# Optimization experiments

Hardware: AMD Instinct MI355X
Metric: run time of the kernel (lower is better)

## Reference

```python
import jax, jax.numpy as jnp
import numpy as np
from jax import lax

# dims (see shape_source)
B, C, H, W = 2, 128, 48, 48
HEADS = 4
G = 4                 # offset_groups = heads
DH = C // HEADS       # 32, dim_head
DF = 4                # downsample_factor
OKS = 6               # offset_kernel_size
PAD = (OKS - DF) // 2 # 1
OFFSET_SCALE = 4.0
CPB_DIM = C // 4      # 32
OD = C // G           # offset_dims = 32


def setup_inputs() -> dict:
    key = jax.random.key(0)
    ks = jax.random.split(key, 12)
    rn = lambda k, shape, s=0.05: jax.random.normal(k, shape, dtype=jnp.float32) * s
    return {
        "x": jax.random.normal(ks[0], (B, C, H, W), dtype=jnp.float32),
        "gamma": jax.random.normal(ks[1], (1,), dtype=jnp.float32),  # nn.Parameter([0.0]); randomized so both paths contribute
        "wq": rn(ks[2], (G, DH, C // G)),    # grouped 1x1 conv, groups=G
        "wk": rn(ks[3], (G, DH, C // G)),
        "wv": rn(ks[4], (G, DH, C // G)),
        "wo": rn(ks[5], (C, C)),             # to_out 1x1 conv
        "bo": jnp.zeros((C,), jnp.float32),
        "w_off_dw": rn(ks[6], (OD, 1, OKS, OKS)),  # depthwise conv k=6 s=4 p=1
        "b_off_dw": jnp.zeros((OD,), jnp.float32),
        "w_off_proj": rn(ks[7], (2, OD)),          # 1x1 conv to 2 offset channels, no bias
        "cpb_w0": rn(ks[8], (2, CPB_DIM), 0.5),
        "cpb_b0": jnp.zeros((CPB_DIM,), jnp.float32),
        "cpb_w1": rn(ks[9], (CPB_DIM, CPB_DIM), 0.2),
        "cpb_b1": jnp.zeros((CPB_DIM,), jnp.float32),
        "cpb_w2": rn(ks[10], (CPB_DIM, HEADS // G), 0.2),
        "cpb_b2": jnp.zeros((HEADS // G,), jnp.float32),
    }


def _bilinear_sample(img, px, py):
    """F.grid_sample(mode='bilinear', padding_mode='zeros') on pixel coords.
    img: (N, Cg, Hi, Wi); px, py: (N, Ho, Wo) -> (N, Cg, Ho, Wo)"""
    N, Cg, Hi, Wi = img.shape
    imgf = img.reshape(N, Cg, Hi * Wi)
    x0 = jnp.floor(px)
    y0 = jnp.floor(py)
    wx1 = px - x0
    wy1 = py - y0

    def corner(xc, yc, w):
        valid = (xc >= 0) & (xc <= Wi - 1) & (yc >= 0) & (yc <= Hi - 1)
        xi = jnp.clip(xc, 0, Wi - 1).astype(jnp.int32)
        yi = jnp.clip(yc, 0, Hi - 1).astype(jnp.int32)
        idx = (yi * Wi + xi).reshape(N, -1)
        vals = jnp.take_along_axis(imgf, idx[:, None, :], axis=2)  # (N,Cg,Ho*Wo)
        return vals * (w * valid).reshape(N, 1, -1)

    out = (corner(x0, y0, (1 - wx1) * (1 - wy1))
           + corner(x0 + 1, y0, wx1 * (1 - wy1))
           + corner(x0, y0 + 1, (1 - wx1) * wy1)
           + corner(x0 + 1, y0 + 1, wx1 * wy1))
    return out.reshape(N, Cg, px.shape[1], px.shape[2])


def _forward(x, gamma, wq, wk, wv, wo, bo, w_off_dw, b_off_dw, w_off_proj,
             cpb_w0, cpb_b0, cpb_w1, cpb_b1, cpb_w2, cpb_b2):
    b = x.shape[0]
    scale = DH ** -0.5
    xg = x.reshape(b, G, C // G, H, W)
    # grouped 1x1 conv -> queries (b, G, DH, H, W); channel layout (g d) == (h d) since G==HEADS
    q = jnp.einsum('bgchw,goc->bgohw', xg, wq)
    gq = q.reshape(b * G, DH, H, W)
    # to_offsets: depthwise conv (k=6, s=4, p=1) -> GELU -> 1x1 to 2ch -> tanh -> *offset_scale
    off = lax.conv_general_dilated(gq, w_off_dw, (DF, DF), [(PAD, PAD), (PAD, PAD)],
                                   feature_group_count=OD,
                                   dimension_numbers=('NCHW', 'OIHW', 'NCHW'))
    off = jax.nn.gelu(off + b_off_dw[None, :, None, None], approximate=False)
    off = jnp.tanh(jnp.einsum('bchw,oc->bohw', off, w_off_proj)) * OFFSET_SCALE  # (bG,2,Hd,Wd)
    Hd, Wd = off.shape[-2], off.shape[-1]
    gy, gx = jnp.meshgrid(jnp.arange(Hd, dtype=jnp.float32),
                          jnp.arange(Wd, dtype=jnp.float32), indexing='ij')
    vg0 = gx[None] + off[:, 0]  # channel 0 = x (meshgrid 'xy' in torch code)
    vg1 = gy[None] + off[:, 1]  # channel 1 = y
    vn0 = 2.0 * vg0 / max(Hd - 1, 1) - 1.0  # normalize_grid (H==W so h/w quirk is moot)
    vn1 = 2.0 * vg1 / max(Wd - 1, 1) - 1.0
    # grid_sample align_corners=False unnormalization: pix = ((u+1)*size - 1)/2
    px = ((vn0 + 1.0) * W - 1.0) / 2.0
    py = ((vn1 + 1.0) * H - 1.0) / 2.0
    kv = _bilinear_sample(xg.reshape(b * G, C // G, H, W), px, py)  # (bG, C/G, Hd, Wd)
    kvg = kv.reshape(b, G, C // G, Hd, Wd)
    k = jnp.einsum('bgchw,goc->bgohw', kvg, wk)
    v = jnp.einsum('bgchw,goc->bgohw', kvg, wv)
    i, j = H * W, Hd * Wd
    qh = q.reshape(b, HEADS, DH, i).transpose(0, 1, 3, 2) * scale  # (b,h,i,d)
    kh = k.reshape(b, HEADS, DH, j).transpose(0, 1, 3, 2)
    vh = v.reshape(b, HEADS, DH, j).transpose(0, 1, 3, 2)
    sim = jnp.einsum('bhid,bhjd->bhij', qh, kh)
    # CPB relative position bias
    gyq, gxq = jnp.meshgrid(jnp.arange(H, dtype=jnp.float32),
                            jnp.arange(W, dtype=jnp.float32), indexing='ij')
    qn0 = 2.0 * gxq / max(H - 1, 1) - 1.0
    qn1 = 2.0 * gyq / max(W - 1, 1) - 1.0
    grid_q = jnp.stack([qn0, qn1], -1).reshape(1, i, 1, 2)
    grid_kv = jnp.stack([vn0, vn1], -1).reshape(b * G, 1, j, 2)
    pos = grid_q - grid_kv                       # (bG, i, j, 2)
    bias = jnp.sign(pos) * jnp.log1p(jnp.abs(pos))
    h1 = jax.nn.relu(bias @ cpb_w0 + cpb_b0)
    h2 = jax.nn.relu(h1 @ cpb_w1 + cpb_b1)
    bias = h2 @ cpb_w2 + cpb_b2                  # (bG, i, j, heads//G)
    bias = bias.reshape(b, G, i, j, HEADS // G).transpose(0, 1, 4, 2, 3).reshape(b, HEADS, i, j)
    attn = jax.nn.softmax(sim + bias, axis=-1)
    outh = jnp.einsum('bhij,bhjd->bhid', attn, vh)
    out = outh.transpose(0, 1, 3, 2).reshape(b, C, H, W)  # 'b h (x y) d -> b (h d) x y'
    attention = jnp.einsum('bchw,oc->bohw', out, wo) + bo[None, :, None, None]
    return gamma[0] * attention + x, attention


def reference(x, gamma, wq, wk, wv, wo, bo, w_off_dw, b_off_dw, w_off_proj,
              cpb_w0, cpb_b0, cpb_w1, cpb_b1, cpb_w2, cpb_b2):
    return _forward(x, gamma, wq, wk, wv, wo, bo, w_off_dw, b_off_dw, w_off_proj,
                    cpb_w0, cpb_b0, cpb_w1, cpb_b1, cpb_w2, cpb_b2)
```

## Files before the change

### kernel.cpp

```cpp
#include <hip/hip_runtime.h>
#include <math.h>

#define HWHW 2304
#define JD   144
#define LSP  148

typedef __attribute__((ext_vector_type(8))) short short8;
typedef __attribute__((ext_vector_type(4))) float f32x4;
typedef __attribute__((ext_vector_type(2))) float f32x2;

__device__ inline ushort f2bf(float f) {
  uint u = __float_as_uint(f);
  u += 0x7fffu + ((u >> 16) & 1u);
  return (ushort)(u >> 16);
}
__device__ inline float bf2f(ushort s) { return __uint_as_float((uint)s << 16); }
__device__ inline uint packbf(float hi, float lo) {
  return __builtin_amdgcn_perm(__float_as_uint(hi), __float_as_uint(lo), 0x07060302);
}


__global__ __launch_bounds__(384) void offset_kv_kernel(
    const float* __restrict__ x, const float* __restrict__ wq,
    const float* __restrict__ wdw, const float* __restrict__ bdw,
    const float* __restrict__ wproj, const float* __restrict__ wk,
    const float* __restrict__ wv,
    ushort* __restrict__ ktb, ushort* __restrict__ vtb,
    float* __restrict__ S0g, float* __restrict__ S1g) {
  __shared__ float qs[288][33];
  __shared__ float wdws[36][32];
  __shared__ float wkl[32][33], wvl[32][33];
  __shared__ float kvs[32][13];
  __shared__ float spx[12], spy[12];
  __shared__ float spn0[12], spn1[12];
  int hd = blockIdx.x, bg = blockIdx.y, b = bg >> 2, g = bg & 3;
  int t = threadIdx.x;
  int w = t >> 6, lane = t & 63, lam = lane & 15, quad = lane >> 4;

  {
    int hy = hd * 4 - 1 + w;
    if (hy >= 0 && hy < 48) {
      const float* wqg = wq + (g * 32) * 32;
      float4 wa = *(const float4*)(wqg + lam * 32 + quad * 8);
      float4 wb = *(const float4*)(wqg + lam * 32 + quad * 8 + 4);
      float4 wc = *(const float4*)(wqg + (16 + lam) * 32 + quad * 8);
      float4 wd = *(const float4*)(wqg + (16 + lam) * 32 + quad * 8 + 4);
      union { uint u[4]; short8 s8; } bf0, bf1;
      bf0.u[0] = packbf(wa.y, wa.x); bf0.u[1] = packbf(wa.w, wa.z);
      bf0.u[2] = packbf(wb.y, wb.x); bf0.u[3] = packbf(wb.w, wb.z);
      bf1.u[0] = packbf(wc.y, wc.x); bf1.u[1] = packbf(wc.w, wc.z);
      bf1.u[2] = packbf(wd.y, wd.x); bf1.u[3] = packbf(wd.w, wd.z);
      const float* xg = x + (b * 128 + g * 32) * HWHW + hy * 48;
#pragma unroll
      for (int tt = 0; tt < 3; ++tt) {
        int col = tt * 16 + lam;
        union { uint u[4]; short8 s8; } xa;
#pragma unroll
        for (int j = 0; j < 4; ++j) {
          float x0 = xg[(quad * 8 + 2 * j) * HWHW + col];
          float x1 = xg[(quad * 8 + 2 * j + 1) * HWHW + col];
          xa.u[j] = packbf(x1, x0);
        }
        f32x4 z = {0.f, 0.f, 0.f, 0.f};
        f32x4 d0 = __builtin_amdgcn_mfma_f32_16x16x32_bf16(xa.s8, bf0.s8, z, 0, 0, 0);
        f32x4 d1 = __builtin_amdgcn_mfma_f32_16x16x32_bf16(xa.s8, bf1.s8, z, 0, 0, 0);
        int p = w * 48 + tt * 16 + quad * 4;
#pragma unroll
        for (int r = 0; r < 4; ++r) {
          qs[p + r][lam] = d0[r];
          qs[p + r][16 + lam] = d1[r];
        }
      }
    } else {
#pragma unroll
      for (int tt = 0; tt < 3; ++tt) {
        int p = w * 48 + tt * 16 + quad * 4;
#pragma unroll
        for (int r = 0; r < 4; ++r) {
          qs[p + r][lam] = 0.f;
          qs[p + r][16 + lam] = 0.f;
        }
      }
    }
  }
  for (int u = t; u < 1152; u += 384) wdws[u >> 5][u & 31] = wdw[(u & 31) * 36 + (u >> 5)];
  for (int u = t; u < 1024; u += 384) {
    int d = u >> 5, c = u & 31;
    wkl[d][c] = wk[g * 1024 + u];
    wvl[d][c] = wv[g * 1024 + u];
  }
  __syncthreads();
  {
    int wd = t >> 5, c = t & 31;
    float s = 0.f;
#pragma unroll
    for (int ky = 0; ky < 6; ++ky) {
#pragma unroll
      for (int kx = 0; kx < 6; ++kx) {
        int wx = wd * 4 - 1 + kx;
        if (wx >= 0 && wx < 48)
          s += wdws[ky * 6 + kx][c] * qs[ky * 48 + wx][c];
      }
    }
    s += bdw[c];
    s = 0.5f * s * (1.f + erff(s * 0.70710678118654752f));
    float g0 = wproj[c] * s;
    float g1 = wproj[32 + c] * s;
#pragma unroll
    for (int k = 16; k >= 1; k >>= 1) {
      g0 += __shfl_xor(g0, k, 64);
      g1 += __shfl_xor(g1, k, 64);
    }
    if (c == 0) {
      float off0 = tanhf(g0) * 4.f;
      float off1 = tanhf(g1) * 4.f;
      float n0 = 2.f * ((float)wd + off0) / 11.f - 1.f;
      float n1 = 2.f * ((float)hd + off1) / 11.f - 1.f;
      spn0[wd] = n0;
      spn1[wd] = n1;
      spx[wd] = ((n0 + 1.f) * 48.f - 1.f) * 0.5f;
      spy[wd] = ((n1 + 1.f) * 48.f - 1.f) * 0.5f;
    }
  }
  __syncthreads();
  {
    int j = t >> 5, c = t & 31;
    float fx = spx[j], fy = spy[j];
    float x0 = floorf(fx), y0 = floorf(fy);
    float wx = fx - x0, wy = fy - y0;
    int xi = (int)x0, yi = (int)y0;
    const float* xp = x + (b * 128 + g * 32 + c) * HWHW;
    float v00 = 0.f, v10 = 0.f, v01 = 0.f, v11 = 0.f;
    bool okx0 = (xi >= 0) & (xi < 48), okx1 = (xi + 1 >= 0) & (xi + 1 < 48);
    if (yi >= 0 && yi < 48) {
      if (okx0) v00 = xp[yi * 48 + xi];
      if (okx1) v10 = xp[yi * 48 + xi + 1];
    }
    if (yi + 1 >= 0 && yi + 1 < 48) {
      if (okx0) v01 = xp[(yi + 1) * 48 + xi];
      if (okx1) v11 = xp[(yi + 1) * 48 + xi + 1];
    }
    kvs[c][j] = v00 * (1.f - wx) * (1.f - wy) + v10 * wx * (1.f - wy)
              + v01 * (1.f - wx) * wy + v11 * wx * wy;
  }
  {
#pragma unroll
    for (int it = 0; it < 3; ++it) {
      int u = t + it * 384;
      int tab = u >= 576;
      int idx = tab ? u - 576 : u;
      int ii = idx / 12, wd = idx - ii * 12;
      float qn = (float)ii * (2.f / 47.f) - 1.f;
      float nv = tab ? spn1[wd] : spn0[wd];
      float p = qn - nv;
      float sres = copysignf(__logf(1.f + fabsf(p)), p);
      float* dst = tab ? S1g : S0g;
      dst[bg * 6912 + ii * 144 + hd * 12 + wd] = sres;
    }
  }
  __syncthreads();
  {
    int j = t >> 5, d = t & 31;
    float ak = 0.f, av = 0.f;
#pragma unroll
    for (int c = 0; c < 32; ++c) {
      float val = kvs[c][j];
      ak += wkl[d][c] * val;
      av += wvl[d][c] * val;
    }
    int jg = hd * 12 + j;
    ktb[bg * 4608 + jg * 32 + d] = f2bf(ak);
    vtb[bg * 5120 + d * 160 + jg] = f2bf(av);
  }
  if (hd == 0) {
    for (int u = t; u < 512; u += 384)
      vtb[bg * 5120 + (u >> 4) * 160 + 144 + (u & 15)] = 0;
  }
}

__global__ __launch_bounds__(256) void attn_fused_kernel(
    const float* __restrict__ x, const float* __restrict__ wq,
    const ushort* __restrict__ ktb, const ushort* __restrict__ vtb,
    const float* __restrict__ S0g, const float* __restrict__ S1g,
    const float* __restrict__ w0, const float* __restrict__ b0,
    const float* __restrict__ w1, const float* __restrict__ b1,
    const float* __restrict__ w2, const float* __restrict__ b2,
    ushort* __restrict__ outh) {
  __shared__ __align__(16) char smem[20288];
  float* Ls = (float*)smem;
  float* st0f = (float*)(smem + 9472);
  float* st1f = (float*)(smem + 18688);
  ushort* qbf = (ushort*)(smem + 19264);

  int bg = blockIdx.y, b = bg >> 2, g = bg & 3;
  int i0 = blockIdx.x * 16;
  int t = threadIdx.x;
  int w = t >> 6, lane = t & 63;
  int lam = lane & 15, quad = lane >> 4;

  {
    int iy = i0 / 48;
    int ix0 = i0 - iy * 48;
    const float* S0p = S0g + bg * 6912 + ix0 * 144;
#pragma unroll
    for (int it = 0; it < 9; ++it) st0f[t + it * 256] = S0p[t + it * 256];
    if (t < JD) st1f[t] = S1g[bg * 6912 + iy * 144 + t];
  }

  {
    const float* wqg = wq + (g * 32) * 32;
    float4 wa = *(const float4*)(wqg + lam * 32 + quad * 8);
    float4 wb = *(const float4*)(wqg + lam * 32 + quad * 8 + 4);
    float4 wc = *(const float4*)(wqg + (16 + lam) * 32 + quad * 8);
    float4 wd = *(const float4*)(wqg + (16 + lam) * 32 + quad * 8 + 4);
    union { uint u[4]; short8 s8; } bf0, bf1, xa;
    bf0.u[0] = packbf(wa.y, wa.x); bf0.u[1] = packbf(wa.w, wa.z);
    bf0.u[2] = packbf(wb.y, wb.x); bf0.u[3] = packbf(wb.w, wb.z);
    bf1.u[0] = packbf(wc.y, wc.x); bf1.u[1] = packbf(wc.w, wc.z);
    bf1.u[2] = packbf(wd.y, wd.x); bf1.u[3] = packbf(wd.w, wd.z);
    const float* xg = x + (b * 128 + g * 32) * HWHW + i0;
#pragma unroll
    for (int j = 0; j < 4; ++j) {
      float x0 = xg[(quad * 8 + 2 * j) * HWHW + lam];
      float x1 = xg[(quad * 8 + 2 * j + 1) * HWHW + lam];
      xa.u[j] = packbf(x1, x0);
    }
    f32x4 z = {0.f, 0.f, 0.f, 0.f};
    f32x4 d0 = __builtin_amdgcn_mfma_f32_16x16x32_bf16(xa.s8, bf0.s8, z, 0, 0, 0);
    f32x4 d1 = __builtin_amdgcn_mfma_f32_16x16x32_bf16(xa.s8, bf1.s8, z, 0, 0, 0);
#pragma unroll
    for (int r = 0; r < 4; ++r) {
      qbf[(quad * 4 + r) * 32 + lam] = f2bf(d0[r]);
      qbf[(quad * 4 + r) * 32 + 16 + lam] = f2bf(d1[r]);
    }
  }

  f32x2 w00r2[4], w01r2[4], b0r2[4];
#pragma unroll
  for (int j = 0; j < 4; ++j) {
    int k = quad * 8 + 2 * j;
    w00r2[j] = (f32x2){w0[k], w0[k + 1]};
    w01r2[j] = (f32x2){w0[32 + k], w0[32 + k + 1]};
    b0r2[j]  = (f32x2){b0[k], b0[k + 1]};
  }
  short8 w1f0, w1f1;
#pragma unroll
  for (int j = 0; j < 8; ++j) {
    int k = quad * 8 + j;
    w1f0[j] = (short)f2bf(w1[k * 32 + lam]);
    w1f1[j] = (short)f2bf(w1[k * 32 + 16 + lam]);
  }
  f32x4 zA, zB;
  f32x2 w2A01, w2A23, w2B01, w2B23;
#pragma unroll
  for (int r = 0; r < 4; ++r) {
    zA[r] = b1[quad * 4 + r];
    zB[r] = b1[16 + quad * 4 + r];
  }
  w2A01 = (f32x2){w2[quad * 4], w2[quad * 4 + 1]};
  w2A23 = (f32x2){w2[quad * 4 + 2], w2[quad * 4 + 3]};
  w2B01 = (f32x2){w2[16 + quad * 4], w2[16 + quad * 4 + 1]};
  w2B23 = (f32x2){w2[16 + quad * 4 + 2], w2[16 + quad * 4 + 3]};
  float b2s = b2[0];

  short8 vf[5];
  if (w < 2) {
    const ushort* vb = vtb + bg * 5120 + (w * 16 + lam) * 160;
#pragma unroll
    for (int kb = 0; kb < 5; ++kb)
      vf[kb] = *(const short8*)(vb + kb * 32 + quad * 8);
  }

  __syncthreads();

  const float scale = 0.17677669529663687f;
  {
    short8 aq = *(const short8*)(qbf + lam * 32 + quad * 8);
    const ushort* kb = ktb + bg * 4608;
#pragma unroll 1
    for (int jt = w; jt < 9; jt += 4) {
      short8 bk = *(const short8*)(kb + (jt * 16 + lam) * 32 + quad * 8);
      f32x4 acc = {0.f, 0.f, 0.f, 0.f};
      acc = __builtin_amdgcn_mfma_f32_16x16x32_bf16(aq, bk, acc, 0, 0, 0);
#pragma unroll
      for (int r = 0; r < 4; ++r)
        Ls[(quad * 4 + r) * LSP + jt * 16 + lam] = acc[r] * scale;
    }
  }
  __syncthreads();

  const f32x2 zero2 = {0.f, 0.f};
  int pbase = w * 576;
#pragma unroll 1
  for (int s = 0; s < 9; ++s) {
    float bm[4];
#pragma unroll
    for (int mt = 0; mt < 4; ++mt) {
      int Pm = pbase + s * 64 + mt * 16 + lam;
      float s0 = st0f[Pm];
      int iim = Pm / 144;
      float s1 = st1f[Pm - iim * 144];
      f32x2 s0v = {s0, s0}, s1v = {s1, s1};
      union { uint u[4]; short8 s8; } cvt;
#pragma unroll
      for (int j = 0; j < 4; ++j) {
        f32x2 hv = __builtin_elementwise_max(
            __builtin_elementwise_fma(s0v, w00r2[j],
                __builtin_elementwise_fma(s1v, w01r2[j], b0r2[j])), zero2);
        cvt.u[j] = packbf(hv[1], hv[0]);
      }
      f32x4 dA = __builtin_amdgcn_mfma_f32_16x16x32_bf16(w1f0, cvt.s8, zA, 0, 0, 0);
      f32x4 dB = __builtin_amdgcn_mfma_f32_16x16x32_bf16(w1f1, cvt.s8, zB, 0, 0, 0);
      f32x2 a01 = __builtin_elementwise_max((f32x2){dA[0], dA[1]}, zero2);
      f32x2 a23 = __builtin_elementwise_max((f32x2){dA[2], dA[3]}, zero2);
      f32x2 c01 = __builtin_elementwise_max((f32x2){dB[0], dB[1]}, zero2);
      f32x2 c23 = __builtin_elementwise_max((f32x2){dB[2], dB[3]}, zero2);
      f32x2 av = __builtin_elementwise_fma(a01, w2A01,
                 __builtin_elementwise_fma(a23, w2A23,
                 __builtin_elementwise_fma(c01, w2B01,
                 __builtin_elementwise_fma(c23, w2B23, zero2))));
      float acc = av[0] + av[1];
      acc += __shfl_xor(acc, 16, 64);
      acc += __shfl_xor(acc, 32, 64);
      bm[mt] = acc;
    }
    int P = s * 64 + lane;
    int ii = P / 144, jj = P - ii * 144;
    float biasv = (quad == 0 ? bm[0] : quad == 1 ? bm[1] : quad == 2 ? bm[2] : bm[3]) + b2s;
    Ls[(w * 4 + ii) * LSP + jj] += biasv;
  }
  __syncthreads();

  {
    int row = w * 4 + quad;
    float* Lp = Ls + row * LSP;
    float lv[9];
#pragma unroll
    for (int k = 0; k < 9; ++k) lv[k] = Lp[lam + 16 * k];
    float m = lv[0];
#pragma unroll
    for (int k = 1; k < 9; ++k) m = fmaxf(m, lv[k]);
#pragma unroll
    for (int k = 8; k >= 1; k >>= 1) m = fmaxf(m, __shfl_xor(m, k, 64));
    float e[9], sum = 0.f;
#pragma unroll
    for (int k = 0; k < 9; ++k) { e[k] = __expf(lv[k] - m); sum += e[k]; }
#pragma unroll
    for (int k = 8; k >= 1; k >>= 1) sum += __shfl_xor(sum, k, 64);
    float inv = 1.f / sum;
    ushort* pb = (ushort*)(Lp + 64);
#pragma unroll
    for (int k = 0; k < 9; ++k) pb[lam + 16 * k] = f2bf(e[k] * inv);
    pb[144 + lam] = 0;
  }
  __syncthreads();

  if (w < 2) {
    f32x4 o = {0.f, 0.f, 0.f, 0.f};
    const ushort* pb = (const ushort*)(Ls + lam * LSP + 64);
#pragma unroll
    for (int kb = 0; kb < 5; ++kb) {
      short8 ap = *(const short8*)(pb + kb * 32 + quad * 8);
      o = __builtin_amdgcn_mfma_f32_16x16x32_bf16(ap, vf[kb], o, 0, 0, 0);
    }
#pragma unroll
    for (int r = 0; r < 4; ++r) {
      int ig = i0 + quad * 4 + r;
      outh[((long)b * HWHW + ig) * 128 + g * 32 + w * 16 + lam] = f2bf(o[r]);
    }
  }
}

__global__ __launch_bounds__(256) void out_kernel(
    const ushort* __restrict__ outh, const float* __restrict__ wo,
    const float* __restrict__ bo, const float* __restrict__ x,
    const float* __restrict__ gamma, float* __restrict__ out) {
  int b = blockIdx.y;
  int hw0 = blockIdx.x * 16;
  int oc0 = blockIdx.z * 64;
  int t = threadIdx.x;
  int w = t >> 6, lane = t & 63, lam = lane & 15, quad = lane >> 4;
  const ushort* abase = outh + ((long)b * HWHW + hw0 + lam) * 128 + quad * 8;
  const float* wb0 = wo + (oc0 + w * 16 + lam) * 128 + quad * 8;
  f32x4 acc0 = {0.f, 0.f, 0.f, 0.f};
#pragma unroll
  for (int ks = 0; ks < 4; ++ks) {
    short8 a = *(const short8*)(abase + ks * 32);
    float4 wa = *(const float4*)(wb0 + ks * 32);
    float4 wb = *(const float4*)(wb0 + ks * 32 + 4);
    union { uint u[4]; short8 s8; } p0;
    p0.u[0] = packbf(wa.y, wa.x); p0.u[1] = packbf(wa.w, wa.z);
    p0.u[2] = packbf(wb.y, wb.x); p0.u[3] = packbf(wb.w, wb.z);
    acc0 = __builtin_amdgcn_mfma_f32_16x16x32_bf16(a, p0.s8, acc0, 0, 0, 0);
  }
  float gm = gamma[0];
  float* out0 = out;
  float* out1 = out + 2 * 128 * HWHW;
  {
    int oc = oc0 + w * 16 + lam;
    float bv = bo[oc];
    long base = ((long)(b * 128 + oc)) * HWHW + hw0 + quad * 4;
    float4 xv = *(const float4*)(x + base);
    float4 a1, a0;
    a1.x = acc0[0] + bv; a1.y = acc0[1] + bv; a1.z = acc0[2] + bv; a1.w = acc0[3] + bv;
    a0.x = fmaf(gm, a1.x, xv.x); a0.y = fmaf(gm, a1.y, xv.y);
    a0.z = fmaf(gm, a1.z, xv.z); a0.w = fmaf(gm, a1.w, xv.w);
    *(float4*)(out1 + base) = a1;
    *(float4*)(out0 + base) = a0;
  }
}

extern "C" void kernel_launch(void* const* d_in, const int* in_sizes, int n_in,
                              void* d_out, int out_size, void* d_ws, size_t ws_size,
                              hipStream_t stream) {
  const float* x     = (const float*)d_in[0];
  const float* gamma = (const float*)d_in[1];
  const float* wq    = (const float*)d_in[2];
  const float* wk    = (const float*)d_in[3];
  const float* wv    = (const float*)d_in[4];
  const float* wo    = (const float*)d_in[5];
  const float* bo    = (const float*)d_in[6];
  const float* wdw   = (const float*)d_in[7];
  const float* bdw   = (const float*)d_in[8];
  const float* wproj = (const float*)d_in[9];
  const float* cw0   = (const float*)d_in[10];
  const float* cb0   = (const float*)d_in[11];
  const float* cw1   = (const float*)d_in[12];
  const float* cb1   = (const float*)d_in[13];
  const float* cw2   = (const float*)d_in[14];
  const float* cb2   = (const float*)d_in[15];
  char* wsb = (char*)d_ws;
  ushort* ktb = (ushort*)(wsb + 9216);
  ushort* vtb = (ushort*)(wsb + 82944);
  ushort* outh = (ushort*)(wsb + 164864);
  float* S0g  = (float*)(wsb + 1344512);
  float* S1g  = (float*)(wsb + 1565696);
  float* out  = (float*)d_out;

  offset_kv_kernel<<<dim3(12, 8), 384, 0, stream>>>(x, wq, wdw, bdw, wproj, wk, wv,
                                                    ktb, vtb, S0g, S1g);
  attn_fused_kernel<<<dim3(144, 8), 256, 0, stream>>>(x, wq, ktb, vtb, S0g, S1g,
                                                      cw0, cb0, cw1, cb1, cw2, cb2, outh);
  out_kernel<<<dim3(144, 2, 2), 256, 0, stream>>>(outh, wo, bo, x, gamma, out);
}
```

Baseline: 130.8 us.

## Fuse output projection into attention kernel with one block per spatial tile

Merges the attention kernel and the output 1x1-conv kernel into one 1024-thread block. The block handles all four groups for a 16-pixel tile and keeps the head outputs in shared memory for the projection MFMA. This removes the bf16 intermediate global round trip and one launch. It also drops the softmax-invariant constant bias and reads the offset-grid tables directly from global memory instead of staging them. The risks are fewer, larger blocks, register pressure from the launch bounds, and uncoalesced global reads in the bias MLP loop.

```diff
diff --git a/kernel.cpp b/kernel.cpp
--- a/kernel.cpp
+++ b/kernel.cpp
@@ -178,34 +178,34 @@
   }
 }
 
-__global__ __launch_bounds__(256) void attn_fused_kernel(
+__global__ __launch_bounds__(1024, 8) void attn_out_kernel(
     const float* __restrict__ x, const float* __restrict__ wq,
     const ushort* __restrict__ ktb, const ushort* __restrict__ vtb,
     const float* __restrict__ S0g, const float* __restrict__ S1g,
     const float* __restrict__ w0, const float* __restrict__ b0,
     const float* __restrict__ w1, const float* __restrict__ b1,
-    const float* __restrict__ w2, const float* __restrict__ b2,
-    ushort* __restrict__ outh) {
-  __shared__ __align__(16) char smem[20288];
+    const float* __restrict__ w2,
+    const float* __restrict__ wo, const float* __restrict__ bo,
+    const float* __restrict__ gamma, float* __restrict__ out) {
+  __shared__ __align__(16) char smem[46336];
   float* Ls = (float*)smem;
-  float* st0f = (float*)(smem + 9472);
-  float* st1f = (float*)(smem + 18688);
-  ushort* qbf = (ushort*)(smem + 19264);
-
-  int bg = blockIdx.y, b = bg >> 2, g = bg & 3;
+  ushort* qbf = (ushort*)(smem + 37888);
+  ushort* obf = (ushort*)(smem + 41984);
+
+  int b = blockIdx.y;
   int i0 = blockIdx.x * 16;
   int t = threadIdx.x;
   int w = t >> 6, lane = t & 63;
   int lam = lane & 15, quad = lane >> 4;
-
-  {
-    int iy = i0 / 48;
-    int ix0 = i0 - iy * 48;
-    const float* S0p = S0g + bg * 6912 + ix0 * 144;
-#pragma unroll
-    for (int it = 0; it < 9; ++it) st0f[t + it * 256] = S0p[t + it * 256];
-    if (t < JD) st1f[t] = S1g[bg * 6912 + iy * 144 + t];
-  }
+  int g = w >> 2, sub = w & 3;
+  int bg = b * 4 + g;
+  float* Lsg = Ls + g * 16 * LSP;
+  ushort* qbg = qbf + g * 512;
+
+  int iy = i0 / 48;
+  int ix0 = i0 - iy * 48;
+  const float* S0p = S0g + bg * 6912 + ix0 * 144;
+  const float* S1p = S1g + bg * 6912 + iy * 144;
 
   {
     const float* wqg = wq + (g * 32) * 32;
@@ -230,8 +230,8 @@
     f32x4 d1 = __builtin_amdgcn_mfma_f32_16x16x32_bf16(xa.s8, bf1.s8, z, 0, 0, 0);
 #pragma unroll
     for (int r = 0; r < 4; ++r) {
-      qbf[(quad * 4 + r) * 32 + lam] = f2bf(d0[r]);
-      qbf[(quad * 4 + r) * 32 + 16 + lam] = f2bf(d1[r]);
+      qbg[(quad * 4 + r) * 32 + lam] = f2bf(d0[r]);
+      qbg[(quad * 4 + r) * 32 + 16 + lam] = f2bf(d1[r]);
     }
   }
 
@@ -261,11 +261,10 @@
   w2A23 = (f32x2){w2[quad * 4 + 2], w2[quad * 4 + 3]};
   w2B01 = (f32x2){w2[16 + quad * 4], w2[16 + quad * 4 + 1]};
   w2B23 = (f32x2){w2[16 + quad * 4 + 2], w2[16 + quad * 4 + 3]};
-  float b2s = b2[0];
 
   short8 vf[5];
-  if (w < 2) {
-    const ushort* vb = vtb + bg * 5120 + (w * 16 + lam) * 160;
+  if (sub < 2) {
+    const ushort* vb = vtb + bg * 5120 + (sub * 16 + lam) * 160;
 #pragma unroll
     for (int kb = 0; kb < 5; ++kb)
       vf[kb] = *(const short8*)(vb + kb * 32 + quad * 8);
@@ -275,31 +274,31 @@
 
   const float scale = 0.17677669529663687f;
   {
-    short8 aq = *(const short8*)(qbf + lam * 32 + quad * 8);
+    short8 aq = *(const short8*)(qbg + lam * 32 + quad * 8);
     const ushort* kb = ktb + bg * 4608;
 #pragma unroll 1
-    for (int jt = w; jt < 9; jt += 4) {
+    for (int jt = sub; jt < 9; jt += 4) {
       short8 bk = *(const short8*)(kb + (jt * 16 + lam) * 32 + quad * 8);
       f32x4 acc = {0.f, 0.f, 0.f, 0.f};
       acc = __builtin_amdgcn_mfma_f32_16x16x32_bf16(aq, bk, acc, 0, 0, 0);
 #pragma unroll
       for (int r = 0; r < 4; ++r)
-        Ls[(quad * 4 + r) * LSP + jt * 16 + lam] = acc[r] * scale;
+        Lsg[(quad * 4 + r) * LSP + jt * 16 + lam] = acc[r] * scale;
     }
   }
   __syncthreads();
 
   const f32x2 zero2 = {0.f, 0.f};
-  int pbase = w * 576;
+  int pbase = sub * 576;
 #pragma unroll 1
   for (int s = 0; s < 9; ++s) {
     float bm[4];
 #pragma unroll
     for (int mt = 0; mt < 4; ++mt) {
       int Pm = pbase + s * 64 + mt * 16 + lam;
-      float s0 = st0f[Pm];
+      float s0 = S0p[Pm];
       int iim = Pm / 144;
-      float s1 = st1f[Pm - iim * 144];
+      float s1 = S1p[Pm - iim * 144];
       f32x2 s0v = {s0, s0}, s1v = {s1, s1};
       union { uint u[4]; short8 s8; } cvt;
 #pragma unroll
@@ -326,14 +325,14 @@
     }
     int P = s * 64 + lane;
     int ii = P / 144, jj = P - ii * 144;
-    float biasv = (quad == 0 ? bm[0] : quad == 1 ? bm[1] : quad == 2 ? bm[2] : bm[3]) + b2s;
-    Ls[(w * 4 + ii) * LSP + jj] += biasv;
-  }
-  __syncthreads();
-
-  {
-    int row = w * 4 + quad;
-    float* Lp = Ls + row * LSP;
+    float biasv = (quad == 0 ? bm[0] : quad == 1 ? bm[1] : quad == 2 ? bm[2] : bm[3]);
+    Lsg[(sub * 4 + ii) * LSP + jj] += biasv;
+  }
+  __syncthreads();
+
+  {
+    int row = sub * 4 + quad;
+    float* Lp = Lsg + row * LSP;
     float lv[9];
 #pragma unroll
     for (int k = 0; k < 9; ++k) lv[k] = Lp[lam + 16 * k];
@@ -355,58 +354,49 @@
   }
   __syncthreads();
 
-  if (w < 2) {
+  if (sub < 2) {
     f32x4 o = {0.f, 0.f, 0.f, 0.f};
-    const ushort* pb = (const ushort*)(Ls + lam * LSP + 64);
+    const ushort* pb = (const ushort*)(Lsg + lam * LSP + 64);
 #pragma unroll
     for (int kb = 0; kb < 5; ++kb) {
       short8 ap = *(const short8*)(pb + kb * 32 + quad * 8);
       o = __builtin_amdgcn_mfma_f32_16x16x32_bf16(ap, vf[kb], o, 0, 0, 0);
     }
 #pragma unroll
-    for (int r = 0; r < 4; ++r) {
-      int ig = i0 + quad * 4 + r;
-      outh[((long)b * HWHW + ig) * 128 + g * 32 + w * 16 + lam] = f2bf(o[r]);
-    }
-  }
-}
-
-__global__ __launch_bounds__(256) void out_kernel(
-    const ushort* __restrict__ outh, const float* __restrict__ wo,
-    const float* __restrict__ bo, const float* __restrict__ x,
-    const float* __restrict__ gamma, float* __restrict__ out) {
-  int b = blockIdx.y;
-  int hw0 = blockIdx.x * 16;
-  int oc0 = blockIdx.z * 64;
-  int t = threadIdx.x;
-  int w = t >> 6, lane = t & 63, lam = lane & 15, quad = lane >> 4;
-  const ushort* abase = outh + ((long)b * HWHW + hw0 + lam) * 128 + quad * 8;
-  const float* wb0 = wo + (oc0 + w * 16 + lam) * 128 + quad * 8;
-  f32x4 acc0 = {0.f, 0.f, 0.f, 0.f};
-#pragma unroll
-  for (int ks = 0; ks < 4; ++ks) {
-    short8 a = *(const short8*)(abase + ks * 32);
-    float4 wa = *(const float4*)(wb0 + ks * 32);
-    float4 wb = *(const float4*)(wb0 + ks * 32 + 4);
-    union { uint u[4]; short8 s8; } p0;
-    p0.u[0] = packbf(wa.y, wa.x); p0.u[1] = packbf(wa.w, wa.z);
-    p0.u[2] = packbf(wb.y, wb.x); p0.u[3] = packbf(wb.w, wb.z);
-    acc0 = __builtin_amdgcn_mfma_f32_16x16x32_bf16(a, p0.s8, acc0, 0, 0, 0);
-  }
-  float gm = gamma[0];
-  float* out0 = out;
-  float* out1 = out + 2 * 128 * HWHW;
-  {
-    int oc = oc0 + w * 16 + lam;
+    for (int r = 0; r < 4; ++r)
+      obf[(quad * 4 + r) * 136 + g * 32 + sub * 16 + lam] = f2bf(o[r]);
+  }
+  __syncthreads();
+
+  if (w < 8) {
+    const ushort* abase = obf + lam * 136 + quad * 8;
+    short8 af0 = *(const short8*)(abase);
+    short8 af1 = *(const short8*)(abase + 32);
+    short8 af2 = *(const short8*)(abase + 64);
+    short8 af3 = *(const short8*)(abase + 96);
+    int oc = w * 16 + lam;
+    const float* wb0 = wo + oc * 128 + quad * 8;
+    f32x4 acc0 = {0.f, 0.f, 0.f, 0.f};
+#pragma unroll
+    for (int ks = 0; ks < 4; ++ks) {
+      short8 a = (ks == 0) ? af0 : (ks == 1) ? af1 : (ks == 2) ? af2 : af3;
+      float4 wa = *(const float4*)(wb0 + ks * 32);
+      float4 wb = *(const float4*)(wb0 + ks * 32 + 4);
+      union { uint u[4]; short8 s8; } p0;
+      p0.u[0] = packbf(wa.y, wa.x); p0.u[1] = packbf(wa.w, wa.z);
+      p0.u[2] = packbf(wb.y, wb.x); p0.u[3] = packbf(wb.w, wb.z);
+      acc0 = __builtin_amdgcn_mfma_f32_16x16x32_bf16(a, p0.s8, acc0, 0, 0, 0);
+    }
+    float gm = gamma[0];
     float bv = bo[oc];
-    long base = ((long)(b * 128 + oc)) * HWHW + hw0 + quad * 4;
+    long base = ((long)(b * 128 + oc)) * HWHW + i0 + quad * 4;
     float4 xv = *(const float4*)(x + base);
     float4 a1, a0;
     a1.x = acc0[0] + bv; a1.y = acc0[1] + bv; a1.z = acc0[2] + bv; a1.w = acc0[3] + bv;
     a0.x = fmaf(gm, a1.x, xv.x); a0.y = fmaf(gm, a1.y, xv.y);
     a0.z = fmaf(gm, a1.z, xv.z); a0.w = fmaf(gm, a1.w, xv.w);
-    *(float4*)(out1 + base) = a1;
-    *(float4*)(out0 + base) = a0;
+    *(float4*)(out + 2 * 128 * HWHW + base) = a1;
+    *(float4*)(out + base) = a0;
   }
 }
 
@@ -428,18 +418,16 @@
   const float* cw1   = (const float*)d_in[12];
   const float* cb1   = (const float*)d_in[13];
   const float* cw2   = (const float*)d_in[14];
-  const float* cb2   = (const float*)d_in[15];
   char* wsb = (char*)d_ws;
   ushort* ktb = (ushort*)(wsb + 9216);
   ushort* vtb = (ushort*)(wsb + 82944);
-  ushort* outh = (ushort*)(wsb + 164864);
   float* S0g  = (float*)(wsb + 1344512);
   float* S1g  = (float*)(wsb + 1565696);
   float* out  = (float*)d_out;
 
   offset_kv_kernel<<<dim3(12, 8), 384, 0, stream>>>(x, wq, wdw, bdw, wproj, wk, wv,
                                                     ktb, vtb, S0g, S1g);
-  attn_fused_kernel<<<dim3(144, 8), 256, 0, stream>>>(x, wq, ktb, vtb, S0g, S1g,
-                                                      cw0, cb0, cw1, cb1, cw2, cb2, outh);
-  out_kernel<<<dim3(144, 2, 2), 256, 0, stream>>>(outh, wo, bo, x, gamma, out);
+  attn_out_kernel<<<dim3(144, 2), 1024, 0, stream>>>(x, wq, ktb, vtb, S0g, S1g,
+                                                     cw0, cb0, cw1, cb1, cw2,
+                                                     wo, bo, gamma, out);
 }
```

Result: slower. 394.5 us (+201.7%).
